# Optimization experiments

Hardware: AMD Instinct MI355X
Metric: run time of the kernel (lower is better)

The kernel has to match this reference:

```python
import jax, jax.numpy as jnp
import numpy as np

IN_FEATURES = 4096
OUT_FEATURES = 4096  # % 16 == 0, so pad_out = 0
BATCH, SEQ = 4, 2048


def setup_inputs() -> dict:
    key = jax.random.key(0)
    k_x, k_w, k_b = jax.random.split(key, 3)
    # int8 activations and weights (W8A8)
    x = jax.random.randint(k_x, (BATCH, SEQ, IN_FEATURES), -128, 128, dtype=jnp.int32).astype(jnp.int8)
    # weight stored as (in_features, out_features), matching qlinear.weight layout
    weight = jax.random.randint(k_w, (IN_FEATURES, OUT_FEATURES), -128, 128, dtype=jnp.int32).astype(jnp.int8)
    # a: scalar input scale; b: per-output-channel dequant/requant scale
    a = jnp.full((1, 1), 0.0123, dtype=jnp.float32)
    b = jax.random.uniform(k_b, (1, OUT_FEATURES), dtype=jnp.float32, minval=0.001, maxval=0.02)
    return {"x": x, "weight": weight, "a": a, "b": b}


def reference(x, weight, a, b):
    # x: [B, S, K] int8; weight: [K, N] int8; a: [1,1] f32; b: [1,N] f32
    x_shape = x.shape
    x2d = x.reshape(-1, x_shape[-1])
    acc = jnp.matmul(x2d, weight, preferred_element_type=jnp.int32)
    # fused dequant (scalar a) + per-channel requant (b), round-to-nearest, saturate to int8
    y_f = acc.astype(jnp.float32) * a * b  # [T, N]
    y = jnp.clip(jnp.round(y_f), -128.0, 127.0).astype(jnp.int8)
    return y.reshape(*x_shape[:-1], -1)
```

## Files before the change

kernel.cpp:

```cpp
#include <hip/hip_runtime.h>
#include <stdint.h>

#define M_DIM 8192
#define N_DIM 4096
#define K_DIM 4096
#define BM 128
#define BN 128
#define BK 64

typedef int v4i __attribute__((ext_vector_type(4)));
typedef unsigned u32;

__device__ __forceinline__ void gll16(const void* g, void* l) {
  __builtin_amdgcn_global_load_lds(
      (const __attribute__((address_space(1))) void*)g,
      (__attribute__((address_space(3))) void*)l, 16, 0, 0);
}

__device__ __forceinline__ u32 pack4(const int4 v) {
  return (v.x & 0xffu) | ((v.y & 0xffu) << 8) | ((v.z & 0xffu) << 16) |
         ((u32)(v.w & 0xffu) << 24);
}

__device__ __forceinline__ bool hdr_is_i32(const int* __restrict__ X, int tid,
                                           int* ok) {
  if (tid == 0) *ok = 1;
  __syncthreads();
  int good = 1;
  for (int i = tid; i < 1024; i += 256) {
    const int w = X[i];
    good &= (w == (int)(int8_t)(w & 0xff));
  }
  if (!good) atomicAnd(ok, 0);
  __syncthreads();
  return *ok != 0;
}

__global__ __launch_bounds__(256) void detect_i32(const int* __restrict__ X,
                                                  u32* __restrict__ flag) {
  __shared__ int ok;
  const bool i32 = hdr_is_i32(X, threadIdx.x, &ok);
  if (threadIdx.x == 0) *flag = i32 ? 1u : 0u;
}

__global__ __launch_bounds__(256) void pack_x_f(const void* __restrict__ Xin,
                                                u32* __restrict__ out) {
  __shared__ int ok;
  const bool i32 = hdr_is_i32((const int*)Xin, threadIdx.x, &ok);
  const int base = blockIdx.x * 1024 + threadIdx.x;
  if (i32) {
    const int4* in = (const int4*)Xin;
#pragma unroll
    for (int j = 0; j < 4; ++j) {
      const int idx = base + j * 256;
      out[idx] = pack4(in[idx]);
    }
  } else {
    const u32* in = (const u32*)Xin;
#pragma unroll
    for (int j = 0; j < 4; ++j) {
      const int idx = base + j * 256;
      out[idx] = in[idx];
    }
  }
}

__global__ __launch_bounds__(256) void packT_w_f(const void* __restrict__ Wv,
                                                 int8_t* __restrict__ WT,
                                                 const int* __restrict__ Xhdr) {
  __shared__ u32 lds[64 * 21];
  __shared__ int ok;
  const int tid = threadIdx.x;
  const bool i32 = hdr_is_i32(Xhdr, tid, &ok);
  const int tk = blockIdx.x & 63;
  const int tn = blockIdx.x >> 6;
  const int k0 = tk * 64, n0 = tn * 64;

#pragma unroll
  for (int j = 0; j < 4; ++j) {
    const int id = j * 256 + tid;
    const int k = id >> 4, c = id & 15;
    u32 word;
    if (i32) {
      const int4 v =
          *(const int4*)((const int*)Wv + (size_t)(k0 + k) * N_DIM + n0 + c * 4);
      word = pack4(v);
    } else {
      word = *(const u32*)((const int8_t*)Wv + (size_t)(k0 + k) * N_DIM + n0 +
                           c * 4);
    }
    lds[k * 21 + c] = word;
  }
  __syncthreads();
  const int kd = tid & 15, nq = tid >> 4;
  const u32 d0 = lds[(kd * 4 + 0) * 21 + nq];
  const u32 d1 = lds[(kd * 4 + 1) * 21 + nq];
  const u32 d2 = lds[(kd * 4 + 2) * 21 + nq];
  const u32 d3 = lds[(kd * 4 + 3) * 21 + nq];
  u32* outp = (u32*)WT;
#pragma unroll
  for (int i = 0; i < 4; ++i) {
    const u32 e = ((d0 >> (8 * i)) & 0xffu) | (((d1 >> (8 * i)) & 0xffu) << 8) |
                  (((d2 >> (8 * i)) & 0xffu) << 16) |
                  (((d3 >> (8 * i)) & 0xffu) << 24);
    const int n = n0 + nq * 4 + i;
    outp[(size_t)n * (K_DIM / 4) + (k0 / 4) + kd] = e;
  }
}

__device__ __forceinline__ void epilogue(const v4i acc[4][4], float a,
                                         const float* __restrict__ bScale,
                                         int* __restrict__ Y, int bm, int bn,
                                         int wm, int wn, int quad, int l16) {
  const int nBase = bn * BN + wn * 64 + l16;
  float bs[4];
#pragma unroll
  for (int ni = 0; ni < 4; ++ni) bs[ni] = bScale[nBase + ni * 16];
#pragma unroll
  for (int mi = 0; mi < 4; ++mi) {
    const int m0 = bm * BM + wm * 64 + mi * 16 + quad * 4;
#pragma unroll
    for (int r = 0; r < 4; ++r) {
      int* row = Y + (size_t)(m0 + r) * N_DIM + nBase;
#pragma unroll
      for (int ni = 0; ni < 4; ++ni) {
        float v = ((float)acc[mi][ni][r] * a) * bs[ni];
        v = rintf(v);
        v = fminf(fmaxf(v, -128.f), 127.f);
        row[ni * 16] = (int)v;
      }
    }
  }
}

__global__ __launch_bounds__(512, 2) void gemm_256(
    const int8_t* __restrict__ X, const int8_t* __restrict__ WT,
    const float* __restrict__ aScale, const float* __restrict__ bScale,
    int* __restrict__ Y) {
  __shared__ __align__(16) int8_t lds[131072];
  const int tid = threadIdx.x;
  const int lane = tid & 63;
  const int wave = tid >> 6;
  const int quad = lane >> 4, l16 = lane & 15;
  const int wm = wave >> 2, wn = wave & 3;

  const int swzb = (blockIdx.x & 7) * 64 + (blockIdx.x >> 3);
  const int bn = swzb & 15, bm = swzb >> 4;

  const int clog = (((tid & 3) ^ ((tid >> 3) & 3)) << 4);
  const int pc = quad ^ ((l16 >> 1) & 3);

  const int8_t* xa = X + (size_t)(bm * 256 + (tid >> 2)) * K_DIM + clog;
  const int8_t* xb = WT + (size_t)(bn * 256 + (tid >> 2)) * K_DIM + clog;
  int8_t* ldsA = lds + tid * 16;
  int8_t* ldsB = lds + 65536 + tid * 16;
  const int8_t* aBase = lds + (wm * 128 + l16) * 64 + pc * 16;
  const int8_t* bBase = lds + 65536 + (wn * 64 + l16) * 64 + pc * 16;

  v4i acc[8][4] = {};

#pragma unroll
  for (int t = 0; t < 3; ++t) {
    gll16(xa + t * 64, ldsA + t * 16384);
    gll16(xa + (size_t)128 * K_DIM + t * 64, ldsA + t * 16384 + 8192);
    gll16(xb + t * 64, ldsB + t * 16384);
    gll16(xb + (size_t)128 * K_DIM + t * 64, ldsB + t * 16384 + 8192);
  }
  asm volatile("s_waitcnt vmcnt(8)" ::: "memory");
  __builtin_amdgcn_s_barrier();

  for (int g = 0; g < 64; ++g) {
    const int soff = (g & 3) << 14;
    const int poff = ((g + 3) & 3) << 14;
    if (g <= 60) {
      const int8_t* sa = xa + (size_t)(g + 3) * 64;
      const int8_t* sb = xb + (size_t)(g + 3) * 64;
      gll16(sa, ldsA + poff);
      gll16(sa + (size_t)128 * K_DIM, ldsA + poff + 8192);
      gll16(sb, ldsB + poff);
      gll16(sb + (size_t)128 * K_DIM, ldsB + poff + 8192);
    }
    v4i bf[4], af[4], ag[4];
#pragma unroll
    for (int i = 0; i < 4; ++i) bf[i] = *(const v4i*)(bBase + soff + i * 1024);
#pragma unroll
    for (int i = 0; i < 4; ++i) af[i] = *(const v4i*)(aBase + soff + i * 1024);
    __builtin_amdgcn_s_setprio(1);
#pragma unroll
    for (int mi = 0; mi < 4; ++mi)
#pragma unroll
      for (int ni = 0; ni < 4; ++ni)
        acc[mi][ni] = __builtin_amdgcn_mfma_i32_16x16x64_i8(
            af[mi], bf[ni], acc[mi][ni], 0, 0, 0);
#pragma unroll
    for (int i = 0; i < 4; ++i)
      ag[i] = *(const v4i*)(aBase + soff + 4096 + i * 1024);
#pragma unroll
    for (int mi = 0; mi < 4; ++mi)
#pragma unroll
      for (int ni = 0; ni < 4; ++ni)
        acc[4 + mi][ni] = __builtin_amdgcn_mfma_i32_16x16x64_i8(
            ag[mi], bf[ni], acc[4 + mi][ni], 0, 0, 0);
    __builtin_amdgcn_s_setprio(0);
    if (g <= 60)
      asm volatile("s_waitcnt vmcnt(8)" ::: "memory");
    else if (g == 61)
      asm volatile("s_waitcnt vmcnt(4)" ::: "memory");
    else
      asm volatile("s_waitcnt vmcnt(0)" ::: "memory");
    __builtin_amdgcn_s_barrier();
  }

  const float a = aScale[0];
  const int nBase = bn * 256 + wn * 64 + l16;
  float bs[4];
#pragma unroll
  for (int ni = 0; ni < 4; ++ni) bs[ni] = bScale[nBase + ni * 16];
#pragma unroll
  for (int mi = 0; mi < 8; ++mi) {
    const int m0 = bm * 256 + wm * 128 + mi * 16 + quad * 4;
#pragma unroll
    for (int r = 0; r < 4; ++r) {
      int* row = Y + (size_t)(m0 + r) * N_DIM + nBase;
#pragma unroll
      for (int ni = 0; ni < 4; ++ni) {
        float v = ((float)acc[mi][ni][r] * a) * bs[ni];
        v = rintf(v);
        v = fminf(fmaxf(v, -128.f), 127.f);
        row[ni * 16] = (int)v;
      }
    }
  }
}

__global__ __launch_bounds__(256) void gemm_inA(
    const void* __restrict__ Xv, const int8_t* __restrict__ WT,
    const float* __restrict__ aScale, const float* __restrict__ bScale,
    int* __restrict__ Y, const u32* __restrict__ flag) {
  __shared__ __align__(16) int8_t As[BM * BK];
  __shared__ __align__(16) int8_t Bs[BN * BK];
  const bool i32 = (*flag != 0);
  const int tid = threadIdx.x;
  const int lane = tid & 63, wave = tid >> 6;
  const int quad = lane >> 4, l16 = lane & 15;
  const int wm = wave & 1, wn = wave >> 1;
  const int bn = blockIdx.x & 31;
  const int bm = blockIdx.x >> 5;

  const int r0 = tid >> 2;
  const int c0 = (tid & 3) * 16;
  const int8_t* Bg0 = WT + (size_t)(bn * BN + r0) * K_DIM + c0;
  const int8_t* Bg1 = Bg0 + (size_t)64 * K_DIM;
  int8_t* Al0 = As + tid * 16;
  int8_t* Al1 = Al0 + 4096;
  int8_t* Bl0 = Bs + tid * 16;
  int8_t* Bl1 = Bl0 + 4096;

  v4i acc[4][4] = {};
  const int8_t* aLds = As + (wm * 64 + l16) * BK + quad * 16;
  const int8_t* bLds = Bs + (wn * 64 + l16) * BK + quad * 16;

  if (i32) {
    const int* Xg0 = (const int*)Xv + (size_t)(bm * BM + r0) * K_DIM + c0;
    const int* Xg1 = Xg0 + (size_t)64 * K_DIM;
    for (int k0 = 0; k0 < K_DIM; k0 += BK) {
      gll16(Bg0 + k0, Bl0);
      gll16(Bg1 + k0, Bl1);
      const int4* p0 = (const int4*)(Xg0 + k0);
      const int4* p1 = (const int4*)(Xg1 + k0);
      uint4 w0, w1;
      w0.x = pack4(p0[0]); w0.y = pack4(p0[1]);
      w0.z = pack4(p0[2]); w0.w = pack4(p0[3]);
      w1.x = pack4(p1[0]); w1.y = pack4(p1[1]);
      w1.z = pack4(p1[2]); w1.w = pack4(p1[3]);
      *(uint4*)Al0 = w0;
      *(uint4*)Al1 = w1;
      __syncthreads();
      v4i af[4], bf[4];
#pragma unroll
      for (int i = 0; i < 4; ++i) af[i] = *(const v4i*)(aLds + i * 16 * BK);
#pragma unroll
      for (int i = 0; i < 4; ++i) bf[i] = *(const v4i*)(bLds + i * 16 * BK);
#pragma unroll
      for (int mi = 0; mi < 4; ++mi)
#pragma unroll
        for (int ni = 0; ni < 4; ++ni)
          acc[mi][ni] = __builtin_amdgcn_mfma_i32_16x16x64_i8(
              af[mi], bf[ni], acc[mi][ni], 0, 0, 0);
      __syncthreads();
    }
  } else {
    const int8_t* Ag0 = (const int8_t*)Xv + (size_t)(bm * BM + r0) * K_DIM + c0;
    const int8_t* Ag1 = Ag0 + (size_t)64 * K_DIM;
    for (int k0 = 0; k0 < K_DIM; k0 += BK) {
      gll16(Ag0 + k0, Al0);
      gll16(Ag1 + k0, Al1);
      gll16(Bg0 + k0, Bl0);
      gll16(Bg1 + k0, Bl1);
      __syncthreads();
      v4i af[4], bf[4];
#pragma unroll
      for (int i = 0; i < 4; ++i) af[i] = *(const v4i*)(aLds + i * 16 * BK);
#pragma unroll
      for (int i = 0; i < 4; ++i) bf[i] = *(const v4i*)(bLds + i * 16 * BK);
#pragma unroll
      for (int mi = 0; mi < 4; ++mi)
#pragma unroll
        for (int ni = 0; ni < 4; ++ni)
          acc[mi][ni] = __builtin_amdgcn_mfma_i32_16x16x64_i8(
              af[mi], bf[ni], acc[mi][ni], 0, 0, 0);
      __syncthreads();
    }
  }
  epilogue(acc, aScale[0], bScale, Y, bm, bn, wm, wn, quad, l16);
}

extern "C" void kernel_launch(void* const* d_in, const int* in_sizes, int n_in,
                              void* d_out, int out_size, void* d_ws,
                              size_t ws_size, hipStream_t stream) {
  const void* Xv = d_in[0];
  const void* Wv = d_in[1];
  const float* a = (const float*)d_in[2];
  const float* b = (const float*)d_in[3];
  int* Y = (int*)d_out;

  const size_t xB = (size_t)M_DIM * K_DIM;
  const size_t wB = (size_t)N_DIM * K_DIM;

  if (ws_size >= xB + wB + 64) {
    int8_t* Xp = (int8_t*)d_ws;
    int8_t* WT = (int8_t*)d_ws + xB;
    pack_x_f<<<(M_DIM * K_DIM / 4) / 1024, 256, 0, stream>>>(Xv, (u32*)Xp);
    packT_w_f<<<(K_DIM / 64) * (N_DIM / 64), 256, 0, stream>>>(Wv, WT,
                                                               (const int*)Xv);
    gemm_256<<<(M_DIM / 256) * (N_DIM / 256), 512, 0, stream>>>(Xp, WT, a, b,
                                                                Y);
  } else if (ws_size >= wB + 64) {
    int8_t* WT = (int8_t*)d_ws;
    u32* flag = (u32*)((int8_t*)d_ws + wB);
    detect_i32<<<1, 256, 0, stream>>>((const int*)Xv, flag);
    packT_w_f<<<(K_DIM / 64) * (N_DIM / 64), 256, 0, stream>>>(Wv, WT,
                                                               (const int*)Xv);
    gemm_inA<<<(M_DIM / BM) * (N_DIM / BN), 256, 0, stream>>>(Xv, WT, a, b, Y,
                                                              flag);
  } else {
    int8_t* WT = (int8_t*)d_ws;
    u32* flag = (u32*)((int8_t*)d_ws + (ws_size >= wB + 4 ? wB : 0));
    detect_i32<<<1, 256, 0, stream>>>((const int*)Xv, flag);
    packT_w_f<<<(K_DIM / 64) * (N_DIM / 64), 256, 0, stream>>>(Wv, WT,
                                                               (const int*)Xv);
    gemm_inA<<<(M_DIM / BM) * (N_DIM / BN), 256, 0, stream>>>(Xv, WT, a, b, Y,
                                                              flag);
  }
}
```

Measured before the change: 407.1 us.

## Prefetch next k-step LDS fragments into registers during current MFMA step

Restructures the main k-loop into a ping-pong register pipeline: the A and B fragments for step g+1 are read from LDS before the MFMAs of step g run, with a sched_barrier to keep that ordering. Global-to-LDS waits tighten from vmcnt(8) to vmcnt(4) so the next stage is resident one step earlier, and the final barrier is dropped. The aim is to hide LDS read latency behind MFMA work. The cost is extra VGPRs for the second fragment set under a 512-thread, 2-block launch bound, plus less slack on global loads.

Result: no change. 399.5 us (-1.9%).

```diff
diff --git a/kernel.cpp b/kernel.cpp
--- a/kernel.cpp
+++ b/kernel.cpp
@@ -133,6 +133,54 @@
   }
 }
 
+__device__ __forceinline__ void rd4(v4i* f, const int8_t* base, int off) {
+#pragma unroll
+  for (int i = 0; i < 4; ++i) f[i] = *(const v4i*)(base + off + i * 1024);
+}
+
+__device__ __forceinline__ void mfma16(v4i acc[8][4], int row, const v4i* a,
+                                       const v4i* b) {
+#pragma unroll
+  for (int mi = 0; mi < 4; ++mi)
+#pragma unroll
+    for (int ni = 0; ni < 4; ++ni)
+      acc[row + mi][ni] = __builtin_amdgcn_mfma_i32_16x16x64_i8(
+          a[mi], b[ni], acc[row + mi][ni], 0, 0, 0);
+}
+
+__device__ __forceinline__ void kstep(
+    int g, const int8_t* xa, const int8_t* xb, int8_t* ldsA, int8_t* ldsB,
+    const int8_t* aBase, const int8_t* bBase, v4i afP[4], v4i bfP[4],
+    v4i afQ[4], v4i bfQ[4], v4i acc[8][4]) {
+  const int soff = (g & 3) << 14;
+  if (g <= 60) {
+    const int poff = ((g + 3) & 3) << 14;
+    const int8_t* sa = xa + (size_t)(g + 3) * 64;
+    const int8_t* sb = xb + (size_t)(g + 3) * 64;
+    gll16(sa, ldsA + poff);
+    gll16(sa + (size_t)128 * K_DIM, ldsA + poff + 8192);
+    gll16(sb, ldsB + poff);
+    gll16(sb + (size_t)128 * K_DIM, ldsB + poff + 8192);
+  }
+  if (g <= 62) {
+    const int qoff = ((g + 1) & 3) << 14;
+    rd4(bfQ, bBase, qoff);
+    rd4(afQ, aBase, qoff);
+  }
+  __builtin_amdgcn_sched_barrier(0);
+  __builtin_amdgcn_s_setprio(1);
+  mfma16(acc, 0, afP, bfP);
+  v4i ag[4];
+  rd4(ag, aBase, soff + 4096);
+  mfma16(acc, 4, ag, bfP);
+  __builtin_amdgcn_s_setprio(0);
+  if (g <= 60)
+    asm volatile("s_waitcnt vmcnt(4)" ::: "memory");
+  else if (g == 61)
+    asm volatile("s_waitcnt vmcnt(0)" ::: "memory");
+  if (g <= 61) __builtin_amdgcn_s_barrier();
+}
+
 __global__ __launch_bounds__(512, 2) void gemm_256(
     const int8_t* __restrict__ X, const int8_t* __restrict__ WT,
     const float* __restrict__ aScale, const float* __restrict__ bScale,
@@ -166,49 +214,16 @@
     gll16(xb + t * 64, ldsB + t * 16384);
     gll16(xb + (size_t)128 * K_DIM + t * 64, ldsB + t * 16384 + 8192);
   }
-  asm volatile("s_waitcnt vmcnt(8)" ::: "memory");
+  asm volatile("s_waitcnt vmcnt(4)" ::: "memory");
   __builtin_amdgcn_s_barrier();
 
-  for (int g = 0; g < 64; ++g) {
-    const int soff = (g & 3) << 14;
-    const int poff = ((g + 3) & 3) << 14;
-    if (g <= 60) {
-      const int8_t* sa = xa + (size_t)(g + 3) * 64;
-      const int8_t* sb = xb + (size_t)(g + 3) * 64;
-      gll16(sa, ldsA + poff);
-      gll16(sa + (size_t)128 * K_DIM, ldsA + poff + 8192);
-      gll16(sb, ldsB + poff);
-      gll16(sb + (size_t)128 * K_DIM, ldsB + poff + 8192);
-    }
-    v4i bf[4], af[4], ag[4];
-#pragma unroll
-    for (int i = 0; i < 4; ++i) bf[i] = *(const v4i*)(bBase + soff + i * 1024);
-#pragma unroll
-    for (int i = 0; i < 4; ++i) af[i] = *(const v4i*)(aBase + soff + i * 1024);
-    __builtin_amdgcn_s_setprio(1);
-#pragma unroll
-    for (int mi = 0; mi < 4; ++mi)
-#pragma unroll
-      for (int ni = 0; ni < 4; ++ni)
-        acc[mi][ni] = __builtin_amdgcn_mfma_i32_16x16x64_i8(
-            af[mi], bf[ni], acc[mi][ni], 0, 0, 0);
-#pragma unroll
-    for (int i = 0; i < 4; ++i)
-      ag[i] = *(const v4i*)(aBase + soff + 4096 + i * 1024);
-#pragma unroll
-    for (int mi = 0; mi < 4; ++mi)
-#pragma unroll
-      for (int ni = 0; ni < 4; ++ni)
-        acc[4 + mi][ni] = __builtin_amdgcn_mfma_i32_16x16x64_i8(
-            ag[mi], bf[ni], acc[4 + mi][ni], 0, 0, 0);
-    __builtin_amdgcn_s_setprio(0);
-    if (g <= 60)
-      asm volatile("s_waitcnt vmcnt(8)" ::: "memory");
-    else if (g == 61)
-      asm volatile("s_waitcnt vmcnt(4)" ::: "memory");
-    else
-      asm volatile("s_waitcnt vmcnt(0)" ::: "memory");
-    __builtin_amdgcn_s_barrier();
+  v4i afP[4], bfP[4], afQ[4], bfQ[4];
+  rd4(bfP, bBase, 0);
+  rd4(afP, aBase, 0);
+
+  for (int g = 0; g < 64; g += 2) {
+    kstep(g, xa, xb, ldsA, ldsB, aBase, bBase, afP, bfP, afQ, bfQ, acc);
+    kstep(g + 1, xa, xb, ldsA, ldsB, aBase, bBase, afQ, bfQ, afP, bfP, acc);
   }
 
   const float a = aScale[0];
```

## Shrink LDS pipeline to double buffering to fit more blocks per CU

Applied to the files above, without the earlier changes.

Reduces the shared-memory ring from four stages (128KB) to two stages (64KB) and raises the launch-bounds minimum blocks hint from 2 to 4, so more workgroups can be resident per CU. The prefetch distance drops from three tiles ahead to one, and every iteration now waits for all outstanding loads before the barrier. The intent is to trade deep software pipelining for higher occupancy hiding latency. The risk is exposed global-load latency, and register pressure from the 4-block hint may force spills given 128 accumulator registers per thread. It also factors the LDS reads and MFMA blocks into helper functions.

Measured after the change: 1.330 ms. 227% more time.

```diff
diff --git a/kernel.cpp b/kernel.cpp
--- a/kernel.cpp
+++ b/kernel.cpp
@@ -133,11 +133,26 @@
   }
 }
 
-__global__ __launch_bounds__(512, 2) void gemm_256(
+__device__ __forceinline__ void rd4(v4i* f, const int8_t* base, int off) {
+#pragma unroll
+  for (int i = 0; i < 4; ++i) f[i] = *(const v4i*)(base + off + i * 1024);
+}
+
+__device__ __forceinline__ void mfma16(v4i acc[8][4], int row, const v4i* a,
+                                       const v4i* b) {
+#pragma unroll
+  for (int mi = 0; mi < 4; ++mi)
+#pragma unroll
+    for (int ni = 0; ni < 4; ++ni)
+      acc[row + mi][ni] = __builtin_amdgcn_mfma_i32_16x16x64_i8(
+          a[mi], b[ni], acc[row + mi][ni], 0, 0, 0);
+}
+
+__global__ __launch_bounds__(512, 4) void gemm_256(
     const int8_t* __restrict__ X, const int8_t* __restrict__ WT,
     const float* __restrict__ aScale, const float* __restrict__ bScale,
     int* __restrict__ Y) {
-  __shared__ __align__(16) int8_t lds[131072];
+  __shared__ __align__(16) int8_t lds[65536];
   const int tid = threadIdx.x;
   const int lane = tid & 63;
   const int wave = tid >> 6;
@@ -153,61 +168,39 @@
   const int8_t* xa = X + (size_t)(bm * 256 + (tid >> 2)) * K_DIM + clog;
   const int8_t* xb = WT + (size_t)(bn * 256 + (tid >> 2)) * K_DIM + clog;
   int8_t* ldsA = lds + tid * 16;
-  int8_t* ldsB = lds + 65536 + tid * 16;
+  int8_t* ldsB = lds + 32768 + tid * 16;
   const int8_t* aBase = lds + (wm * 128 + l16) * 64 + pc * 16;
-  const int8_t* bBase = lds + 65536 + (wn * 64 + l16) * 64 + pc * 16;
+  const int8_t* bBase = lds + 32768 + (wn * 64 + l16) * 64 + pc * 16;
 
   v4i acc[8][4] = {};
 
-#pragma unroll
-  for (int t = 0; t < 3; ++t) {
-    gll16(xa + t * 64, ldsA + t * 16384);
-    gll16(xa + (size_t)128 * K_DIM + t * 64, ldsA + t * 16384 + 8192);
-    gll16(xb + t * 64, ldsB + t * 16384);
-    gll16(xb + (size_t)128 * K_DIM + t * 64, ldsB + t * 16384 + 8192);
-  }
-  asm volatile("s_waitcnt vmcnt(8)" ::: "memory");
+  gll16(xa, ldsA);
+  gll16(xa + (size_t)128 * K_DIM, ldsA + 8192);
+  gll16(xb, ldsB);
+  gll16(xb + (size_t)128 * K_DIM, ldsB + 8192);
+  asm volatile("s_waitcnt vmcnt(0)" ::: "memory");
   __builtin_amdgcn_s_barrier();
 
   for (int g = 0; g < 64; ++g) {
-    const int soff = (g & 3) << 14;
-    const int poff = ((g + 3) & 3) << 14;
-    if (g <= 60) {
-      const int8_t* sa = xa + (size_t)(g + 3) * 64;
-      const int8_t* sb = xb + (size_t)(g + 3) * 64;
+    const int soff = (g & 1) << 14;
+    if (g < 63) {
+      const int poff = ((g + 1) & 1) << 14;
+      const int8_t* sa = xa + (size_t)(g + 1) * 64;
+      const int8_t* sb = xb + (size_t)(g + 1) * 64;
       gll16(sa, ldsA + poff);
       gll16(sa + (size_t)128 * K_DIM, ldsA + poff + 8192);
       gll16(sb, ldsB + poff);
       gll16(sb + (size_t)128 * K_DIM, ldsB + poff + 8192);
     }
     v4i bf[4], af[4], ag[4];
-#pragma unroll
-    for (int i = 0; i < 4; ++i) bf[i] = *(const v4i*)(bBase + soff + i * 1024);
-#pragma unroll
-    for (int i = 0; i < 4; ++i) af[i] = *(const v4i*)(aBase + soff + i * 1024);
+    rd4(bf, bBase, soff);
+    rd4(af, aBase, soff);
     __builtin_amdgcn_s_setprio(1);
-#pragma unroll
-    for (int mi = 0; mi < 4; ++mi)
-#pragma unroll
-      for (int ni = 0; ni < 4; ++ni)
-        acc[mi][ni] = __builtin_amdgcn_mfma_i32_16x16x64_i8(
-            af[mi], bf[ni], acc[mi][ni], 0, 0, 0);
-#pragma unroll
-    for (int i = 0; i < 4; ++i)
-      ag[i] = *(const v4i*)(aBase + soff + 4096 + i * 1024);
-#pragma unroll
-    for (int mi = 0; mi < 4; ++mi)
-#pragma unroll
-      for (int ni = 0; ni < 4; ++ni)
-        acc[4 + mi][ni] = __builtin_amdgcn_mfma_i32_16x16x64_i8(
-            ag[mi], bf[ni], acc[4 + mi][ni], 0, 0, 0);
+    mfma16(acc, 0, af, bf);
+    rd4(ag, aBase, soff + 4096);
+    mfma16(acc, 4, ag, bf);
     __builtin_amdgcn_s_setprio(0);
-    if (g <= 60)
-      asm volatile("s_waitcnt vmcnt(8)" ::: "memory");
-    else if (g == 61)
-      asm volatile("s_waitcnt vmcnt(4)" ::: "memory");
-    else
-      asm volatile("s_waitcnt vmcnt(0)" ::: "memory");
+    asm volatile("s_waitcnt vmcnt(0)" ::: "memory");
     __builtin_amdgcn_s_barrier();
   }
 
```
